# Optimization experiments

Hardware: AMD Instinct MI355X
Metric: run time of the kernel (lower is better)

## Reference

```python
import jax, jax.numpy as jnp
import numpy as np

TEMPERATURE = 0.1
EPS = 1e-8  # torch cosine_similarity default eps


def _similarity_matrix(left, right):
    # C[i, j] = cosine_similarity(left[i], right[j]) with torch-style eps clamp
    ln = jnp.linalg.norm(left, axis=-1)   # [B]
    rn = jnp.linalg.norm(right, axis=-1)  # [B]
    dots = left @ right.T                 # [B, B]
    denom = jnp.maximum(ln[:, None] * rn[None, :], EPS)
    cos = dots / denom
    # Original builds only the strict upper triangle + diagonal of C, then
    # mirrors the upper triangle: S = triu(C, 1) + diag(C) + triu(C, 1).T
    upper = jnp.triu(cos, k=1)
    return upper + jnp.diag(jnp.diag(cos)) + upper.T


def reference(left_features, right_features):
    sims = _similarity_matrix(left_features, right_features) / TEMPERATURE
    # cross_entropy(sims, eye) == mean_i( -log_softmax(sims)[i, i] )
    logp = jax.nn.log_softmax(sims, axis=-1)
    return -jnp.mean(jnp.diagonal(logp))


def setup_inputs() -> dict:
    key = jax.random.key(0)
    k1, k2 = jax.random.split(key)
    B, D = 4096, 1024
    return {
        "left_features": jax.random.normal(k1, (B, D), dtype=jnp.float32),
        "right_features": jax.random.normal(k2, (B, D), dtype=jnp.float32),
    }
```

## Files before the change

kernel.cpp:

```cpp
#include <hip/hip_runtime.h>

typedef unsigned short u16;
typedef __bf16 bf16x8 __attribute__((ext_vector_type(8)));
typedef float f32x4 __attribute__((ext_vector_type(4)));

#define B_DIM 4096
#define D_DIM 1024
#define TT    32
#define NT    16

#define GLOAD_LDS16(g, l)                                            \
    __builtin_amdgcn_global_load_lds(                                \
        (const __attribute__((address_space(1))) void*)(g),          \
        (__attribute__((address_space(3))) void*)(l), 16, 0, 0)

__device__ inline u16 f2bf(float f) {
    union { float f; unsigned u; } x; x.f = f;
    unsigned u = x.u;
    return (u16)((u + 0x7fffu + ((u >> 16) & 1u)) >> 16);
}

__device__ inline float wave_reduce_sum(float v) {
    #pragma unroll
    for (int off = 32; off > 0; off >>= 1) v += __shfl_down(v, off);
    return v;
}

__global__ __launch_bounds__(256) void norm_convert_kernel(
        const float* __restrict__ L, const float* __restrict__ R,
        u16* __restrict__ Lbf, u16* __restrict__ Rbf,
        float* __restrict__ ln, float* __restrict__ rn,
        float* __restrict__ rowsum) {
    if (blockIdx.x == 0) {
        #pragma unroll
        for (int i = 0; i < B_DIM / 256; ++i)
            rowsum[threadIdx.x + i * 256] = 0.f;
    }
    const int wave = threadIdx.x >> 6;
    const int lane = threadIdx.x & 63;
    int g = blockIdx.x * 4 + wave;
    const float* in; u16* outb; float* nout; int row;
    if (g < B_DIM) { in = L; outb = Lbf; nout = ln; row = g; }
    else           { in = R; outb = Rbf; nout = rn; row = g - B_DIM; }

    const float4* r4 = reinterpret_cast<const float4*>(in + (size_t)row * D_DIM);
    ushort4* o4 = reinterpret_cast<ushort4*>(outb + (size_t)row * D_DIM);
    float ss = 0.f;
    #pragma unroll
    for (int c = 0; c < 4; ++c) {
        float4 v = r4[lane + 64 * c];
        ss += v.x * v.x + v.y * v.y + v.z * v.z + v.w * v.w;
        ushort4 o;
        o.x = f2bf(v.x); o.y = f2bf(v.y); o.z = f2bf(v.z); o.w = f2bf(v.w);
        o4[lane + 64 * c] = o;
    }
    #pragma unroll
    for (int off = 32; off > 0; off >>= 1) ss += __shfl_xor(ss, off);
    if (lane == 0) nout[row] = sqrtf(ss);
}

__global__ __launch_bounds__(256) void gemm_fused_kernel(
        const u16* __restrict__ Lbf, const u16* __restrict__ Rbf,
        const float* __restrict__ ln, const float* __restrict__ rn,
        float* __restrict__ rowsum, float* __restrict__ diag) {
    __shared__ __align__(16) u16 Ls[2][128 * 64];
    __shared__ __align__(16) u16 Rs[2][128 * 64];

    int bid = (int)blockIdx.x;
    int swz = (bid & 7) * 66 + (bid >> 3);
    int b = swz;
    int ti = 0;
    while (b >= TT - ti) { b -= TT - ti; ++ti; }
    const int tj = ti + b;
    const int brow = ti * 128;
    const int bcol = tj * 128;
    const bool diagblk = (ti == tj);

    const int tid  = threadIdx.x;
    const int lane = tid & 63;
    const int wave = tid >> 6;
    const int wr   = wave >> 1;
    const int wc   = wave & 1;
    const int fr   = lane & 15;

    const int l8 = lane >> 3;
    const int c8 = lane & 7;
    size_t gA[4], gB[4];
    int ldsOff[4];
    #pragma unroll
    for (int s = 0; s < 4; ++s) {
        int row = (wave * 4 + s) * 8 + l8;
        int chunk = c8 ^ (row & 7);
        gA[s] = (size_t)(brow + row) * D_DIM + chunk * 8;
        gB[s] = (size_t)(bcol + row) * D_DIM + chunk * 8;
        ldsOff[s] = (wave * 4 + s) * 512;
    }

#define STAGE(buf, k0)                                               \
    do {                                                             \
        _Pragma("unroll")                                            \
        for (int s = 0; s < 4; ++s) {                                \
            GLOAD_LDS16(Lbf + gA[s] + (k0), &Ls[buf][ldsOff[s]]);    \
            GLOAD_LDS16(Rbf + gB[s] + (k0), &Rs[buf][ldsOff[s]]);    \
        }                                                            \
    } while (0)

    f32x4 acc[4][4] = {};

#define COMPUTE(buf)                                                  \
    do {                                                              \
        _Pragma("unroll")                                             \
        for (int kk = 0; kk < 2; ++kk) {                              \
            bf16x8 af[4], bfr[4];                                     \
            _Pragma("unroll")                                         \
            for (int m = 0; m < 4; ++m) {                             \
                int row = wr * 64 + m * 16 + fr;                      \
                int cs = ((kk << 2) | (lane >> 4)) ^ (row & 7);       \
                af[m] = *reinterpret_cast<const bf16x8*>(             \
                    &Ls[buf][row * 64 + cs * 8]);                     \
            }                                                         \
            _Pragma("unroll")                                         \
            for (int n = 0; n < 4; ++n) {                             \
                int row = wc * 64 + n * 16 + fr;                      \
                int cs = ((kk << 2) | (lane >> 4)) ^ (row & 7);       \
                bfr[n] = *reinterpret_cast<const bf16x8*>(            \
                    &Rs[buf][row * 64 + cs * 8]);                     \
            }                                                         \
            _Pragma("unroll")                                         \
            for (int m = 0; m < 4; ++m)                               \
                _Pragma("unroll")                                     \
                for (int n = 0; n < 4; ++n)                           \
                    acc[m][n] = __builtin_amdgcn_mfma_f32_16x16x32_bf16( \
                        af[m], bfr[n], acc[m][n], 0, 0, 0);           \
        }                                                             \
    } while (0)

    STAGE(0, 0);

    int cur = 0;
    for (int t = 0; t < NT; ++t) {
        if (t + 1 < NT) {
            STAGE(cur ^ 1, (t + 1) * 64);
            asm volatile("s_waitcnt vmcnt(8)" ::: "memory");
        } else {
            asm volatile("s_waitcnt vmcnt(0)" ::: "memory");
        }
        __builtin_amdgcn_s_barrier();
        asm volatile("" ::: "memory");
        COMPUTE(cur);
        asm volatile("" ::: "memory");
        __builtin_amdgcn_s_barrier();
        cur ^= 1;
    }

    const int fcol  = lane & 15;
    const int frow0 = (lane >> 4) * 4;

    float rnj[4];
    #pragma unroll
    for (int n = 0; n < 4; ++n)
        rnj[n] = rn[bcol + wc * 64 + n * 16 + fcol];

    float colacc[4] = {0.f, 0.f, 0.f, 0.f};

    #pragma unroll
    for (int m = 0; m < 4; ++m) {
        #pragma unroll
        for (int r = 0; r < 4; ++r) {
            const int i = brow + wr * 64 + m * 16 + frow0 + r;
            const float lni = ln[i];
            float rowacc = 0.f;
            #pragma unroll
            for (int n = 0; n < 4; ++n) {
                const int j = bcol + wc * 64 + n * 16 + fcol;
                const float denom = fmaxf(lni * rnj[n], 1e-8f);
                const float v = acc[m][n][r] * 10.0f / denom;
                if (diagblk && i == j) diag[i] = v;
                const float e = __expf(v);
                if (i <= j) rowacc += e;
                if (i < j)  colacc[n] += e;
            }
            rowacc += __shfl_xor(rowacc, 1);
            rowacc += __shfl_xor(rowacc, 2);
            rowacc += __shfl_xor(rowacc, 4);
            rowacc += __shfl_xor(rowacc, 8);
            if (fcol == 0) atomicAdd(&rowsum[i], rowacc);
        }
    }
    #pragma unroll
    for (int n = 0; n < 4; ++n) {
        float c = colacc[n];
        c += __shfl_xor(c, 16);
        c += __shfl_xor(c, 32);
        if (lane < 16) {
            const int j = bcol + wc * 64 + n * 16 + fcol;
            atomicAdd(&rowsum[j], c);
        }
    }
#undef STAGE
#undef COMPUTE
}

__global__ __launch_bounds__(1024) void final_loss_kernel(
        const float* __restrict__ rowsum, const float* __restrict__ diag,
        float* __restrict__ out) {
    float s = 0.f;
    for (int i = threadIdx.x; i < B_DIM; i += 1024)
        s += logf(rowsum[i]) - diag[i];
    __shared__ float red[16];
    float w = wave_reduce_sum(s);
    if ((threadIdx.x & 63) == 0) red[threadIdx.x >> 6] = w;
    __syncthreads();
    if (threadIdx.x == 0) {
        float tot = 0.f;
        #pragma unroll
        for (int k = 0; k < 16; ++k) tot += red[k];
        out[0] = tot / (float)B_DIM;
    }
}

extern "C" void kernel_launch(void* const* d_in, const int* in_sizes, int n_in,
                              void* d_out, int out_size, void* d_ws, size_t ws_size,
                              hipStream_t stream) {
    const float* L = (const float*)d_in[0];
    const float* R = (const float*)d_in[1];

    char* ws = (char*)d_ws;
    size_t o = 0;
    u16* Lbf   = (u16*)(ws + o);   o += (size_t)B_DIM * D_DIM * sizeof(u16);
    u16* Rbf   = (u16*)(ws + o);   o += (size_t)B_DIM * D_DIM * sizeof(u16);
    float* ln  = (float*)(ws + o); o += (size_t)B_DIM * sizeof(float);
    float* rn  = (float*)(ws + o); o += (size_t)B_DIM * sizeof(float);
    float* rs  = (float*)(ws + o); o += (size_t)B_DIM * sizeof(float);
    float* dg  = (float*)(ws + o); o += (size_t)B_DIM * sizeof(float);

    norm_convert_kernel<<<2 * B_DIM / 4, 256, 0, stream>>>(L, R, Lbf, Rbf, ln, rn, rs);

    const int nblocks = TT * (TT + 1) / 2;
    gemm_fused_kernel<<<nblocks, 256, 0, stream>>>(Lbf, Rbf, ln, rn, rs, dg);

    final_loss_kernel<<<1, 1024, 0, stream>>>(rs, dg, (float*)d_out);
}
```

Baseline: 131.7 us.

## Shrink GEMM tiles to 64x64 and replace atomics with slot-partitioned partial sums

Reduces the upper-triangular GEMM tile from 128x128 to 64x64, which raises the block count from 528 to 2080 and adds an occupancy hint of 4 blocks per SM. Per-row and per-column exp sums are written to disjoint slots of a 130xB partial buffer instead of being atomically added. Two new reduction kernels replace the single final kernel. This is meant to fix poor load balance and atomic contention, at the cost of lower operand reuse per tile (more global and LDS traffic) and an extra pass over a roughly 2 MB partial buffer.

Result: faster. 127.1 us (-3.5%).

```diff
diff --git a/kernel.cpp b/kernel.cpp
--- a/kernel.cpp
+++ b/kernel.cpp
@@ -6,8 +6,9 @@
 
 #define B_DIM 4096
 #define D_DIM 1024
-#define TT    32
+#define TT    64
 #define NT    16
+#define NSLOT 130
 
 #define GLOAD_LDS16(g, l)                                            \
     __builtin_amdgcn_global_load_lds(                                \
@@ -20,22 +21,10 @@
     return (u16)((u + 0x7fffu + ((u >> 16) & 1u)) >> 16);
 }
 
-__device__ inline float wave_reduce_sum(float v) {
-    #pragma unroll
-    for (int off = 32; off > 0; off >>= 1) v += __shfl_down(v, off);
-    return v;
-}
-
 __global__ __launch_bounds__(256) void norm_convert_kernel(
         const float* __restrict__ L, const float* __restrict__ R,
         u16* __restrict__ Lbf, u16* __restrict__ Rbf,
-        float* __restrict__ ln, float* __restrict__ rn,
-        float* __restrict__ rowsum) {
-    if (blockIdx.x == 0) {
-        #pragma unroll
-        for (int i = 0; i < B_DIM / 256; ++i)
-            rowsum[threadIdx.x + i * 256] = 0.f;
-    }
+        float* __restrict__ ln, float* __restrict__ rn) {
     const int wave = threadIdx.x >> 6;
     const int lane = threadIdx.x & 63;
     int g = blockIdx.x * 4 + wave;
@@ -59,21 +48,19 @@
     if (lane == 0) nout[row] = sqrtf(ss);
 }
 
-__global__ __launch_bounds__(256) void gemm_fused_kernel(
+__global__ __launch_bounds__(256, 4) void gemm_fused_kernel(
         const u16* __restrict__ Lbf, const u16* __restrict__ Rbf,
         const float* __restrict__ ln, const float* __restrict__ rn,
-        float* __restrict__ rowsum, float* __restrict__ diag) {
-    __shared__ __align__(16) u16 Ls[2][128 * 64];
-    __shared__ __align__(16) u16 Rs[2][128 * 64];
+        float* __restrict__ part, float* __restrict__ diag) {
+    __shared__ __align__(16) u16 Ls[2][64 * 64];
+    __shared__ __align__(16) u16 Rs[2][64 * 64];
 
     int bid = (int)blockIdx.x;
-    int swz = (bid & 7) * 66 + (bid >> 3);
-    int b = swz;
-    int ti = 0;
+    int swz = (bid & 7) * 260 + (bid >> 3);
+    int b = swz, ti = 0;
     while (b >= TT - ti) { b -= TT - ti; ++ti; }
     const int tj = ti + b;
-    const int brow = ti * 128;
-    const int bcol = tj * 128;
+    const int brow = ti * 64, bcol = tj * 64;
     const bool diagblk = (ti == tj);
 
     const int tid  = threadIdx.x;
@@ -85,51 +72,51 @@
 
     const int l8 = lane >> 3;
     const int c8 = lane & 7;
-    size_t gA[4], gB[4];
-    int ldsOff[4];
-    #pragma unroll
-    for (int s = 0; s < 4; ++s) {
-        int row = (wave * 4 + s) * 8 + l8;
-        int chunk = c8 ^ (row & 7);
+    size_t gA[2], gB[2];
+    int ldsOff[2];
+    #pragma unroll
+    for (int s = 0; s < 2; ++s) {
+        int row = wave * 16 + s * 8 + l8;
+        int chunk = c8 ^ l8;
         gA[s] = (size_t)(brow + row) * D_DIM + chunk * 8;
         gB[s] = (size_t)(bcol + row) * D_DIM + chunk * 8;
-        ldsOff[s] = (wave * 4 + s) * 512;
+        ldsOff[s] = (wave * 16 + s * 8) * 64;
     }
 
 #define STAGE(buf, k0)                                               \
     do {                                                             \
         _Pragma("unroll")                                            \
-        for (int s = 0; s < 4; ++s) {                                \
+        for (int s = 0; s < 2; ++s) {                                \
             GLOAD_LDS16(Lbf + gA[s] + (k0), &Ls[buf][ldsOff[s]]);    \
             GLOAD_LDS16(Rbf + gB[s] + (k0), &Rs[buf][ldsOff[s]]);    \
         }                                                            \
     } while (0)
 
-    f32x4 acc[4][4] = {};
+    f32x4 acc[2][2] = {};
 
 #define COMPUTE(buf)                                                  \
     do {                                                              \
         _Pragma("unroll")                                             \
         for (int kk = 0; kk < 2; ++kk) {                              \
-            bf16x8 af[4], bfr[4];                                     \
+            bf16x8 af[2], bfr[2];                                     \
             _Pragma("unroll")                                         \
-            for (int m = 0; m < 4; ++m) {                             \
-                int row = wr * 64 + m * 16 + fr;                      \
+            for (int m = 0; m < 2; ++m) {                             \
+                int row = wr * 32 + m * 16 + fr;                      \
                 int cs = ((kk << 2) | (lane >> 4)) ^ (row & 7);       \
                 af[m] = *reinterpret_cast<const bf16x8*>(             \
                     &Ls[buf][row * 64 + cs * 8]);                     \
             }                                                         \
             _Pragma("unroll")                                         \
-            for (int n = 0; n < 4; ++n) {                             \
-                int row = wc * 64 + n * 16 + fr;                      \
+            for (int n = 0; n < 2; ++n) {                             \
+                int row = wc * 32 + n * 16 + fr;                      \
                 int cs = ((kk << 2) | (lane >> 4)) ^ (row & 7);       \
                 bfr[n] = *reinterpret_cast<const bf16x8*>(            \
                     &Rs[buf][row * 64 + cs * 8]);                     \
             }                                                         \
             _Pragma("unroll")                                         \
-            for (int m = 0; m < 4; ++m)                               \
+            for (int m = 0; m < 2; ++m)                               \
                 _Pragma("unroll")                                     \
-                for (int n = 0; n < 4; ++n)                           \
+                for (int n = 0; n < 2; ++n)                           \
                     acc[m][n] = __builtin_amdgcn_mfma_f32_16x16x32_bf16( \
                         af[m], bfr[n], acc[m][n], 0, 0, 0);           \
         }                                                             \
@@ -141,7 +128,7 @@
     for (int t = 0; t < NT; ++t) {
         if (t + 1 < NT) {
             STAGE(cur ^ 1, (t + 1) * 64);
-            asm volatile("s_waitcnt vmcnt(8)" ::: "memory");
+            asm volatile("s_waitcnt vmcnt(4)" ::: "memory");
         } else {
             asm volatile("s_waitcnt vmcnt(0)" ::: "memory");
         }
@@ -156,23 +143,23 @@
     const int fcol  = lane & 15;
     const int frow0 = (lane >> 4) * 4;
 
-    float rnj[4];
-    #pragma unroll
-    for (int n = 0; n < 4; ++n)
-        rnj[n] = rn[bcol + wc * 64 + n * 16 + fcol];
-
-    float colacc[4] = {0.f, 0.f, 0.f, 0.f};
-
-    #pragma unroll
-    for (int m = 0; m < 4; ++m) {
+    float rnj[2];
+    #pragma unroll
+    for (int n = 0; n < 2; ++n)
+        rnj[n] = rn[bcol + wc * 32 + n * 16 + fcol];
+
+    float colacc[2] = {0.f, 0.f};
+
+    #pragma unroll
+    for (int m = 0; m < 2; ++m) {
         #pragma unroll
         for (int r = 0; r < 4; ++r) {
-            const int i = brow + wr * 64 + m * 16 + frow0 + r;
+            const int i = brow + wr * 32 + m * 16 + frow0 + r;
             const float lni = ln[i];
             float rowacc = 0.f;
             #pragma unroll
-            for (int n = 0; n < 4; ++n) {
-                const int j = bcol + wc * 64 + n * 16 + fcol;
+            for (int n = 0; n < 2; ++n) {
+                const int j = bcol + wc * 32 + n * 16 + fcol;
                 const float denom = fmaxf(lni * rnj[n], 1e-8f);
                 const float v = acc[m][n][r] * 10.0f / denom;
                 if (diagblk && i == j) diag[i] = v;
@@ -184,39 +171,48 @@
             rowacc += __shfl_xor(rowacc, 2);
             rowacc += __shfl_xor(rowacc, 4);
             rowacc += __shfl_xor(rowacc, 8);
-            if (fcol == 0) atomicAdd(&rowsum[i], rowacc);
+            if (fcol == 0) part[(size_t)(2 * tj + wc) * B_DIM + i] = rowacc;
         }
     }
     #pragma unroll
-    for (int n = 0; n < 4; ++n) {
+    for (int n = 0; n < 2; ++n) {
         float c = colacc[n];
         c += __shfl_xor(c, 16);
         c += __shfl_xor(c, 32);
         if (lane < 16) {
-            const int j = bcol + wc * 64 + n * 16 + fcol;
-            atomicAdd(&rowsum[j], c);
+            const int j = bcol + wc * 32 + n * 16 + fcol;
+            const int slot = diagblk ? (128 + wr) : (2 * ti + wr);
+            part[(size_t)slot * B_DIM + j] = c;
         }
     }
 #undef STAGE
 #undef COMPUTE
 }
 
-__global__ __launch_bounds__(1024) void final_loss_kernel(
-        const float* __restrict__ rowsum, const float* __restrict__ diag,
-        float* __restrict__ out) {
-    float s = 0.f;
-    for (int i = threadIdx.x; i < B_DIM; i += 1024)
-        s += logf(rowsum[i]) - diag[i];
-    __shared__ float red[16];
-    float w = wave_reduce_sum(s);
-    if ((threadIdx.x & 63) == 0) red[threadIdx.x >> 6] = w;
+__global__ __launch_bounds__(256) void loss_stage1_kernel(
+        const float* __restrict__ part, const float* __restrict__ diag,
+        float* __restrict__ partial) {
+    const int i = blockIdx.x * 256 + threadIdx.x;
+    float rs = 0.f;
+    #pragma unroll 10
+    for (int k = 0; k < NSLOT; ++k)
+        rs += part[(size_t)k * B_DIM + i];
+    float s = logf(rs) - diag[i];
+    #pragma unroll
+    for (int off = 32; off > 0; off >>= 1) s += __shfl_down(s, off);
+    __shared__ float red[4];
+    if ((threadIdx.x & 63) == 0) red[threadIdx.x >> 6] = s;
     __syncthreads();
-    if (threadIdx.x == 0) {
-        float tot = 0.f;
-        #pragma unroll
-        for (int k = 0; k < 16; ++k) tot += red[k];
-        out[0] = tot / (float)B_DIM;
-    }
+    if (threadIdx.x == 0)
+        partial[blockIdx.x] = red[0] + red[1] + red[2] + red[3];
+}
+
+__global__ __launch_bounds__(64) void loss_stage2_kernel(
+        const float* __restrict__ partial, float* __restrict__ out) {
+    float s = (threadIdx.x < 16) ? partial[threadIdx.x] : 0.f;
+    #pragma unroll
+    for (int off = 8; off > 0; off >>= 1) s += __shfl_down(s, off);
+    if (threadIdx.x == 0) out[0] = s / (float)B_DIM;
 }
 
 extern "C" void kernel_launch(void* const* d_in, const int* in_sizes, int n_in,
@@ -227,17 +223,19 @@
 
     char* ws = (char*)d_ws;
     size_t o = 0;
-    u16* Lbf   = (u16*)(ws + o);   o += (size_t)B_DIM * D_DIM * sizeof(u16);
-    u16* Rbf   = (u16*)(ws + o);   o += (size_t)B_DIM * D_DIM * sizeof(u16);
-    float* ln  = (float*)(ws + o); o += (size_t)B_DIM * sizeof(float);
-    float* rn  = (float*)(ws + o); o += (size_t)B_DIM * sizeof(float);
-    float* rs  = (float*)(ws + o); o += (size_t)B_DIM * sizeof(float);
-    float* dg  = (float*)(ws + o); o += (size_t)B_DIM * sizeof(float);
-
-    norm_convert_kernel<<<2 * B_DIM / 4, 256, 0, stream>>>(L, R, Lbf, Rbf, ln, rn, rs);
+    u16* Lbf     = (u16*)(ws + o);   o += (size_t)B_DIM * D_DIM * sizeof(u16);
+    u16* Rbf     = (u16*)(ws + o);   o += (size_t)B_DIM * D_DIM * sizeof(u16);
+    float* ln    = (float*)(ws + o); o += (size_t)B_DIM * sizeof(float);
+    float* rn    = (float*)(ws + o); o += (size_t)B_DIM * sizeof(float);
+    float* part  = (float*)(ws + o); o += (size_t)NSLOT * B_DIM * sizeof(float);
+    float* diag  = (float*)(ws + o); o += (size_t)B_DIM * sizeof(float);
+    float* partial = (float*)(ws + o); o += 16 * sizeof(float);
+
+    norm_convert_kernel<<<2 * B_DIM / 4, 256, 0, stream>>>(L, R, Lbf, Rbf, ln, rn);
 
     const int nblocks = TT * (TT + 1) / 2;
-    gemm_fused_kernel<<<nblocks, 256, 0, stream>>>(Lbf, Rbf, ln, rn, rs, dg);
-
-    final_loss_kernel<<<1, 1024, 0, stream>>>(rs, dg, (float*)d_out);
-}
+    gemm_fused_kernel<<<nblocks, 256, 0, stream>>>(Lbf, Rbf, ln, rn, part, diag);
+
+    loss_stage1_kernel<<<16, 256, 0, stream>>>(part, diag, partial);
+    loss_stage2_kernel<<<1, 64, 0, stream>>>(partial, (float*)d_out);
+}
```
